# Kernel tuning notes

Measured on AMD Instinct MI355X. Metric: run time of the kernel, lower is better.

Reference implementation:

```python
import jax, jax.numpy as jnp
import numpy as np

N, D = 8192, 1024

def setup_inputs() -> dict:
    key = jax.random.key(0)
    ks = jax.random.split(key, 7)
    s = 1.0 / np.sqrt(D)
    return {
        "sent_mat": jax.random.normal(ks[0], (N, D), dtype=jnp.float32),
        "indicator": 0,
        "Wq": jax.random.normal(ks[1], (D, D), dtype=jnp.float32) * s,
        "bq": jax.random.normal(ks[2], (D,), dtype=jnp.float32) * s,
        "Wk": jax.random.normal(ks[3], (D, D), dtype=jnp.float32) * s,
        "bk": jax.random.normal(ks[4], (D,), dtype=jnp.float32) * s,
        "Wv": jax.random.normal(ks[5], (D, D), dtype=jnp.float32) * s,
        "bv": jax.random.normal(ks[6], (D,), dtype=jnp.float32) * s,
    }

def reference(sent_mat, indicator, Wq, bq, Wk, bk, Wv, bv):
    # torch.nn.Linear: y = x @ W.T + b
    Q = sent_mat @ Wq.T + bq            # [N, D]
    K = sent_mat @ Wk.T + bk            # [N, D]
    V = sent_mat @ Wv.T + bv            # [N, D]
    sim = Q @ K.T                       # [N, N]
    if indicator == 0:                  # custom score inversion
        sim = 1.0 - sim
    sim_norm = sim / jnp.sqrt(jnp.asarray(D, dtype=sim.dtype))
    # NOTE: softmax over dim=0 (columns normalized over rows), unconventional
    attn_w = jax.nn.softmax(sim_norm, axis=0)   # [N, N]
    attn_out = attn_w @ V               # [N, D]
    return (attn_out, attn_w)
```

## Files before the change

### kernel.cpp

```cpp
#include <hip/hip_runtime.h>

#define NT 8192
#define DM 1024

typedef unsigned short u16;
typedef __bf16 bf16x8 __attribute__((ext_vector_type(8)));
typedef float f32x4 __attribute__((ext_vector_type(4)));
typedef u16 u16x8 __attribute__((ext_vector_type(8)));

__device__ __forceinline__ u16 f2bf(float f) {
  union { float f; unsigned u; } v; v.f = f;
  unsigned r = v.u + 0x7fffu + ((v.u >> 16) & 1u);
  return (u16)(r >> 16);
}
__device__ __forceinline__ float bf2f(u16 h) {
  union { unsigned u; float f; } v; v.u = ((unsigned)h) << 16;
  return v.f;
}

__device__ __forceinline__ void stage16(const u16* g, u16* lds_wave_uniform) {
  __builtin_amdgcn_global_load_lds(
      (const __attribute__((address_space(1))) unsigned int*)g,
      (__attribute__((address_space(3))) unsigned int*)lds_wave_uniform, 16, 0, 0);
}

__global__ void cvt_all_kernel(const float* __restrict__ X, const float* __restrict__ Wq,
                               const float* __restrict__ Wk, const float* __restrict__ Wv,
                               u16* __restrict__ Xb, u16* __restrict__ Wqb,
                               u16* __restrict__ Wkb, u16* __restrict__ Wvb) {
  const int NX = NT * DM / 4;
  const int NW = DM * DM / 4;
  const int total = NX + 3 * NW;
  int i = blockIdx.x * blockDim.x + threadIdx.x;
  int stride = gridDim.x * blockDim.x;
  for (; i < total; i += stride) {
    const float* src; u16* dst; int j;
    if (i < NX)               { src = X;  dst = Xb;  j = i; }
    else if (i < NX + NW)     { src = Wq; dst = Wqb; j = i - NX; }
    else if (i < NX + 2 * NW) { src = Wk; dst = Wkb; j = i - NX - NW; }
    else                      { src = Wv; dst = Wvb; j = i - NX - 2 * NW; }
    float4 v = reinterpret_cast<const float4*>(src)[j];
    ushort4 o;
    o.x = f2bf(v.x); o.y = f2bf(v.y); o.z = f2bf(v.z); o.w = f2bf(v.w);
    reinterpret_cast<ushort4*>(dst)[j] = o;
  }
}

__global__ __launch_bounds__(512, 2)
void qkt_exp_256(const u16* __restrict__ Q, const u16* __restrict__ Kmat, int K, int lda,
                 u16* __restrict__ E, float* __restrict__ cs,
                 const int* __restrict__ indp) {
  __shared__ u16 AT[2][256 * 64];
  __shared__ u16 BT[2][256 * 64];
  const int t = threadIdx.x;
  const int l = t & 63;
  const int w = t >> 6;
  const int wm = w >> 2;
  const int wn = w & 3;
  const int r16 = l & 15;
  const int half = l >> 4;

  const int gx = gridDim.x;
  const int nwg = gx * gridDim.y;
  int lin = blockIdx.y * gx + blockIdx.x;
  if ((nwg & 7) == 0) lin = (lin & 7) * (nwg >> 3) + (lin >> 3);
  const int bx = lin % gx;
  const int by = lin / gx;
  const size_t brow = (size_t)by * 256;
  const size_t bcol = (size_t)bx * 256;

  const int srow = w * 8 + (l >> 3);
  const int kel = ((l & 7) ^ (l >> 3)) * 8;
  const int ntiles = K >> 6;

  f32x4 acc[8][4] = {};

#pragma unroll
  for (int q = 0; q < 4; ++q) {
    stage16(Q    + (brow + q * 64 + srow) * (size_t)lda + kel, &AT[0][q * 4096 + w * 512]);
    stage16(Kmat + (bcol + q * 64 + srow) * (size_t)lda + kel, &BT[0][q * 4096 + w * 512]);
  }
  __syncthreads();

  for (int tt = 0; tt < ntiles; ++tt) {
    const int cur = tt & 1;
    const int nxt = cur ^ 1;
    const int k1 = (tt + 1) << 6;
    const bool more = (tt + 1 < ntiles);
#pragma unroll
    for (int p = 0; p < 4; ++p) {
      if (p == 0 && more) {
#pragma unroll
        for (int q = 0; q < 4; ++q)
          stage16(Q + (brow + q * 64 + srow) * (size_t)lda + (k1 + kel),
                  &AT[nxt][q * 4096 + w * 512]);
      }
      if (p == 1 && more) {
#pragma unroll
        for (int q = 0; q < 4; ++q)
          stage16(Kmat + (bcol + q * 64 + srow) * (size_t)lda + (k1 + kel),
                  &BT[nxt][q * 4096 + w * 512]);
      }
      bf16x8 af[4][2], bfr[2][2];
#pragma unroll
      for (int m = 0; m < 4; ++m) {
        const int row = wm * 128 + (p >> 1) * 64 + m * 16 + r16;
#pragma unroll
        for (int kk = 0; kk < 2; ++kk) {
          const int slot = (half + 4 * kk) ^ (r16 & 7);
          af[m][kk] = *reinterpret_cast<const bf16x8*>(&AT[cur][row * 64 + slot * 8]);
        }
      }
#pragma unroll
      for (int n = 0; n < 2; ++n) {
        const int row = wn * 64 + (p & 1) * 32 + n * 16 + r16;
#pragma unroll
        for (int kk = 0; kk < 2; ++kk) {
          const int slot = (half + 4 * kk) ^ (r16 & 7);
          bfr[n][kk] = *reinterpret_cast<const bf16x8*>(&BT[cur][row * 64 + slot * 8]);
        }
      }
      __builtin_amdgcn_s_setprio(1);
#pragma unroll
      for (int m = 0; m < 4; ++m)
#pragma unroll
        for (int n = 0; n < 2; ++n)
#pragma unroll
          for (int kk = 0; kk < 2; ++kk)
            acc[(p >> 1) * 4 + m][(p & 1) * 2 + n] = __builtin_amdgcn_mfma_f32_16x16x32_bf16(
                af[m][kk], bfr[n][kk], acc[(p >> 1) * 4 + m][(p & 1) * 2 + n], 0, 0, 0);
      __builtin_amdgcn_s_setprio(0);
      __builtin_amdgcn_sched_barrier(0);
    }
    __syncthreads();
  }

  const bool flip = (*indp == 0);
  const float cexp = 0.045084220027780106f;
  float csum[4] = {0.f, 0.f, 0.f, 0.f};
#pragma unroll
  for (int mg = 0; mg < 8; ++mg) {
#pragma unroll
    for (int ng = 0; ng < 4; ++ng) {
#pragma unroll
      for (int q = 0; q < 4; ++q) {
        float s = acc[mg][ng][q];
        float x = flip ? (1.0f - s) : s;
        float e = exp2f(x * cexp);
        size_t row = brow + wm * 128 + mg * 16 + half * 4 + q;
        size_t col = bcol + wn * 64 + ng * 16 + r16;
        E[row * NT + col] = f2bf(e);
        csum[ng] += e;
      }
    }
  }
#pragma unroll
  for (int ng = 0; ng < 4; ++ng) {
    float s = csum[ng];
    s += __shfl_xor(s, 16);
    s += __shfl_xor(s, 32);
    if (l < 16) atomicAdd(&cs[bcol + wn * 64 + ng * 16 + l], s);
  }
}

template<int EPI>
__global__ __launch_bounds__(512, 4)
void mega_bt(const u16* __restrict__ A, const u16* __restrict__ B, int K,
             int lda, int ldb, int ldo,
             const float* __restrict__ b0, const float* __restrict__ b1,
             const float* __restrict__ csp,
             u16* __restrict__ obf, float* __restrict__ of32) {
  __shared__ u16 AT[3][128 * 32];
  __shared__ u16 BT[3][128 * 32];
  const int t = threadIdx.x;
  const int l = t & 63;
  const int w = t >> 6;
  const int wm = w >> 2;
  const int wn = w & 3;
  const int r16 = l & 15;
  const int half = l >> 4;

  const int gx = gridDim.x;
  const int nwg = gx * gridDim.y;
  int lin = blockIdx.y * gx + blockIdx.x;
  if ((nwg & 7) == 0) lin = (lin & 7) * (nwg >> 3) + (lin >> 3);
  const int bx = lin % gx;
  const int by = lin / gx;
  const size_t brow = (size_t)by * 128;
  const size_t bcol = (size_t)bx * 128;

  const int srow = w * 16 + (l >> 2);
  const int kel = (((l & 3) ^ ((l >> 2) & 3) ^ (((l >> 4) & 1) << 1))) * 8;
  const int nt = K >> 5;
  const int slotk = half ^ (r16 & 3) ^ (((r16 >> 2) & 1) << 1);

  f32x4 acc[4][2] = {};

#define STAGE(tile, buf)                                                              \
  {                                                                                   \
    const int k0_ = (tile) << 5;                                                      \
    stage16(A + (brow + srow) * (size_t)lda + (k0_ + kel), &AT[buf][w * 512]);        \
    stage16(B + (bcol + srow) * (size_t)ldb + (k0_ + kel), &BT[buf][w * 512]);        \
  }

  STAGE(0, 0);
  STAGE(1, 1);

  for (int tt = 0; tt < nt; ++tt) {
    const int cur = tt % 3;
    if (tt < nt - 1) asm volatile("s_waitcnt vmcnt(2)" ::: "memory");
    else             asm volatile("s_waitcnt vmcnt(0)" ::: "memory");
    __builtin_amdgcn_s_barrier();
    __builtin_amdgcn_sched_barrier(0);
    if (tt + 2 < nt) STAGE(tt + 2, (tt + 2) % 3);
    __builtin_amdgcn_sched_barrier(0);

    bf16x8 af[4], bfr[2];
#pragma unroll
    for (int m = 0; m < 4; ++m) {
      const int row = wm * 64 + m * 16 + r16;
      af[m] = *reinterpret_cast<const bf16x8*>(&AT[cur][row * 32 + slotk * 8]);
    }
#pragma unroll
    for (int n = 0; n < 2; ++n) {
      const int row = wn * 32 + n * 16 + r16;
      bfr[n] = *reinterpret_cast<const bf16x8*>(&BT[cur][row * 32 + slotk * 8]);
    }
    __builtin_amdgcn_s_setprio(1);
#pragma unroll
    for (int m = 0; m < 4; ++m)
#pragma unroll
      for (int n = 0; n < 2; ++n)
        acc[m][n] = __builtin_amdgcn_mfma_f32_16x16x32_bf16(af[m], bfr[n], acc[m][n], 0, 0, 0);
    __builtin_amdgcn_s_setprio(0);
  }
#undef STAGE

  if constexpr (EPI == 0) {
    const float* bp = ((bcol >> 10) == 0) ? b0 : b1;
#pragma unroll
    for (int mg = 0; mg < 4; ++mg) {
#pragma unroll
      for (int n = 0; n < 2; ++n) {
        const int cc = wn * 32 + n * 16 + r16;
        const float bv = bp[((int)bcol & 1023) + cc];
#pragma unroll
        for (int q = 0; q < 4; ++q) {
          size_t row = brow + wm * 64 + mg * 16 + half * 4 + q;
          obf[row * (size_t)ldo + bcol + cc] = f2bf(acc[mg][n][q] + bv);
        }
      }
    }
  } else if constexpr (EPI == 4) {
#pragma unroll
    for (int n = 0; n < 2; ++n) {
      const int cc = wn * 32 + n * 16 + r16;
      const float invc = 1.0f / csp[bcol + cc];
#pragma unroll
      for (int mg = 0; mg < 4; ++mg) {
#pragma unroll
        for (int q = 0; q < 4; ++q) {
          size_t row = brow + wm * 64 + mg * 16 + half * 4 + q;
          obf[row * (size_t)ldo + bcol + cc] = f2bf((acc[mg][n][q] + b0[row]) * invc);
        }
      }
    }
  } else {
#pragma unroll
    for (int mg = 0; mg < 4; ++mg) {
#pragma unroll
      for (int n = 0; n < 2; ++n) {
#pragma unroll
        for (int q = 0; q < 4; ++q) {
          size_t row = brow + wm * 64 + mg * 16 + half * 4 + q;
          size_t col = bcol + wn * 32 + n * 16 + r16;
          of32[row * (size_t)ldo + col] = acc[mg][n][q];
        }
      }
    }
  }
}

template<int EPI, int AF32, int BF32>
__global__ __launch_bounds__(256)
void gemm_bt(const void* __restrict__ Av, const void* __restrict__ Bv, int K, int ldo,
             const float* __restrict__ bias, u16* __restrict__ obf,
             float* __restrict__ of32, const int* __restrict__ indp) {
  __shared__ u16 As[128 * 32];
  __shared__ u16 Bs[128 * 32];
  const int t = threadIdx.x;
  const int l = t & 63;
  const int w = t >> 6;
  const int wr = w >> 1;
  const int wc = w & 1;
  const int r16 = l & 15;
  const int half = l >> 4;

  const int gx = gridDim.x;
  const int nwg = gx * gridDim.y;
  int lin = blockIdx.y * gx + blockIdx.x;
  if ((nwg & 7) == 0) lin = (lin & 7) * (nwg >> 3) + (lin >> 3);
  const int bx = lin % gx;
  const int by = lin / gx;

  const size_t brow = (size_t)by * 128;
  const size_t bcol = (size_t)bx * 128;
  const int kel = (l & 3) * 8;
  const int lrow = l >> 2;

  f32x4 acc[4][4] = {};

  for (int k0 = 0; k0 < K; k0 += 32) {
#pragma unroll
    for (int c = 0; c < 2; ++c) {
      const int seg = c * 4 + w;
      const int r = seg * 16 + lrow;
      if constexpr (AF32) {
        const float* ga = (const float*)Av + (brow + r) * (size_t)K + (k0 + kel);
        float4 u0 = *reinterpret_cast<const float4*>(ga);
        float4 u1 = *reinterpret_cast<const float4*>(ga + 4);
        u16x8 o;
        o[0] = f2bf(u0.x); o[1] = f2bf(u0.y); o[2] = f2bf(u0.z); o[3] = f2bf(u0.w);
        o[4] = f2bf(u1.x); o[5] = f2bf(u1.y); o[6] = f2bf(u1.z); o[7] = f2bf(u1.w);
        *reinterpret_cast<u16x8*>(&As[seg * 512 + l * 8]) = o;
      } else {
        const u16* ga = (const u16*)Av + (brow + r) * (size_t)K + (k0 + kel);
        stage16(ga, &As[seg * 512]);
      }
      if constexpr (BF32) {
        const float* gb = (const float*)Bv + (bcol + r) * (size_t)K + (k0 + kel);
        float4 u0 = *reinterpret_cast<const float4*>(gb);
        float4 u1 = *reinterpret_cast<const float4*>(gb + 4);
        u16x8 o;
        o[0] = f2bf(u0.x); o[1] = f2bf(u0.y); o[2] = f2bf(u0.z); o[3] = f2bf(u0.w);
        o[4] = f2bf(u1.x); o[5] = f2bf(u1.y); o[6] = f2bf(u1.z); o[7] = f2bf(u1.w);
        *reinterpret_cast<u16x8*>(&Bs[seg * 512 + l * 8]) = o;
      } else {
        const u16* gb = (const u16*)Bv + (bcol + r) * (size_t)K + (k0 + kel);
        stage16(gb, &Bs[seg * 512]);
      }
    }
    __syncthreads();
    bf16x8 af[4], bfv[4];
#pragma unroll
    for (int m = 0; m < 4; ++m)
      af[m] = *reinterpret_cast<const bf16x8*>(&As[(wr * 64 + m * 16 + r16) * 32 + half * 8]);
#pragma unroll
    for (int n = 0; n < 4; ++n)
      bfv[n] = *reinterpret_cast<const bf16x8*>(&Bs[(wc * 64 + n * 16 + r16) * 32 + half * 8]);
#pragma unroll
    for (int m = 0; m < 4; ++m)
#pragma unroll
      for (int n = 0; n < 4; ++n)
        acc[m][n] = __builtin_amdgcn_mfma_f32_16x16x32_bf16(af[m], bfv[n], acc[m][n], 0, 0, 0);
    __syncthreads();
  }

  const int crow0 = wr * 64 + half * 4;
  const int ccol0 = wc * 64 + r16;

  if constexpr (EPI == 0) {
#pragma unroll
    for (int m = 0; m < 4; ++m) {
#pragma unroll
      for (int n = 0; n < 4; ++n) {
        const int cc = ccol0 + n * 16;
        const float bv = bias[bcol + cc];
#pragma unroll
        for (int q = 0; q < 4; ++q) {
          size_t idx = (brow + crow0 + m * 16 + q) * (size_t)ldo + (bcol + cc);
          obf[idx] = f2bf(acc[m][n][q] + bv);
        }
      }
    }
  } else if constexpr (EPI == 1) {
    const bool flip = (*indp == 0);
    const float cexp = 0.045084220027780106f;
#pragma unroll
    for (int m = 0; m < 4; ++m) {
#pragma unroll
      for (int n = 0; n < 4; ++n) {
        const int cc = ccol0 + n * 16;
#pragma unroll
        for (int q = 0; q < 4; ++q) {
          float s = acc[m][n][q];
          float x = flip ? (1.0f - s) : s;
          size_t idx = (brow + crow0 + m * 16 + q) * (size_t)ldo + (bcol + cc);
          of32[idx] = exp2f(x * cexp);
        }
      }
    }
  } else {
#pragma unroll
    for (int m = 0; m < 4; ++m) {
#pragma unroll
      for (int n = 0; n < 4; ++n) {
        const int cc = ccol0 + n * 16;
#pragma unroll
        for (int q = 0; q < 4; ++q) {
          size_t idx = (brow + crow0 + m * 16 + q) * (size_t)ldo + (bcol + cc);
          of32[idx] = acc[m][n][q];
        }
      }
    }
  }
}

__global__ void colsum_kernel(const float* __restrict__ E, float* __restrict__ cs) {
  const int col = blockIdx.x * 256 + threadIdx.x;
  const int r0 = blockIdx.y * 256;
  float s = 0.f;
  for (int r = r0; r < r0 + 256; ++r)
    s += E[(size_t)r * NT + col];
  atomicAdd(&cs[col], s);
}

__global__ void norm_kernel(float* __restrict__ w, const float* __restrict__ cs, int n4) {
  int i = blockIdx.x * blockDim.x + threadIdx.x;
  int stride = gridDim.x * blockDim.x;
  for (; i < n4; i += stride) {
    float4 v = reinterpret_cast<float4*>(w)[i];
    int j4 = i & (NT / 4 - 1);
    float4 c = reinterpret_cast<const float4*>(cs)[j4];
    v.x /= c.x; v.y /= c.y; v.z /= c.z; v.w /= c.w;
    reinterpret_cast<float4*>(w)[i] = v;
  }
}

__global__ void norm_bf16_kernel(const u16* __restrict__ e, float* __restrict__ w,
                                 const float* __restrict__ cs, int n4) {
  int i = blockIdx.x * blockDim.x + threadIdx.x;
  int stride = gridDim.x * blockDim.x;
  for (; i < n4; i += stride) {
    ushort4 ev = reinterpret_cast<const ushort4*>(e)[i];
    int j4 = i & (NT / 4 - 1);
    float4 c = reinterpret_cast<const float4*>(cs)[j4];
    float4 v;
    v.x = bf2f(ev.x) / c.x;
    v.y = bf2f(ev.y) / c.y;
    v.z = bf2f(ev.z) / c.z;
    v.w = bf2f(ev.w) / c.w;
    reinterpret_cast<float4*>(w)[i] = v;
  }
}

__global__ void vt_kernel(const u16* __restrict__ Vb, const float* __restrict__ cs,
                          u16* __restrict__ Vt) {
  __shared__ u16 tile[64][65];
  const int jb = blockIdx.x * 64;
  const int db = blockIdx.y * 64;
  const int t = threadIdx.x;
  {
    const int d = t & 63;
    const int j0 = t >> 6;
    for (int jj = j0; jj < 64; jj += 4)
      tile[jj][d] = Vb[(size_t)(jb + jj) * DM + db + d];
  }
  __syncthreads();
  {
    const int j = t & 63;
    const int d0 = t >> 6;
    const float inv = cs ? (1.0f / cs[jb + j]) : 1.0f;
    for (int dd = d0; dd < 64; dd += 4) {
      u16 raw = tile[j][dd];
      Vt[(size_t)(db + dd) * NT + jb + j] = cs ? f2bf(bf2f(raw) * inv) : raw;
    }
  }
}

extern "C" void kernel_launch(void* const* d_in, const int* in_sizes, int n_in,
                              void* d_out, int out_size, void* d_ws, size_t ws_size,
                              hipStream_t stream) {
  const float* X  = (const float*)d_in[0];
  const int* indp = (const int*)d_in[1];
  const float* Wq = (const float*)d_in[2];
  const float* bq = (const float*)d_in[3];
  const float* Wk = (const float*)d_in[4];
  const float* bk = (const float*)d_in[5];
  const float* Wv = (const float*)d_in[6];
  const float* bv = (const float*)d_in[7];

  float* attn_out = (float*)d_out;
  float* attn_w   = (float*)d_out + (size_t)NT * DM;

  const size_t EB_BYTES = (size_t)NT * NT * 2;
  const size_t QKV_BYTES = (size_t)NT * DM * 2;
  const size_t need_fast = EB_BYTES + 4 * QKV_BYTES + NT * 4;

  if (ws_size >= need_fast) {
    char* ws = (char*)d_ws;
    u16* Eb  = (u16*)ws;
    u16* QKb = (u16*)(ws + EB_BYTES);
    u16* Vt  = QKb + (size_t)NT * 2048;
    u16* Xb  = Vt + (size_t)DM * NT;
    u16* Wvb = Xb + (size_t)NT * DM;
    float* cs = (float*)(Wvb + (size_t)DM * DM);
    u16* Wqkb = Eb;
    u16* Wqb = Wqkb;
    u16* Wkb = Wqkb + (size_t)DM * DM;

    cvt_all_kernel<<<2048, 256, 0, stream>>>(X, Wq, Wk, Wv, Xb, Wqb, Wkb, Wvb);

    mega_bt<0><<<dim3(2048 / 128, NT / 128), 512, 0, stream>>>(
        Xb, Wqkb, DM, DM, DM, 2048, bq, bk, nullptr, QKb, nullptr);

    hipMemsetAsync(cs, 0, NT * sizeof(float), stream);
    qkt_exp_256<<<dim3(NT / 256, NT / 256), 512, 0, stream>>>(
        QKb, QKb + 1024, DM, 2048, Eb, cs, indp);

    mega_bt<4><<<dim3(NT / 128, DM / 128), 512, 0, stream>>>(
        Wvb, Xb, DM, DM, DM, NT, bv, nullptr, cs, Vt, nullptr);

    mega_bt<2><<<dim3(DM / 128, NT / 128), 512, 0, stream>>>(
        Eb, Vt, NT, NT, NT, DM, nullptr, nullptr, nullptr, nullptr, attn_out);

    norm_bf16_kernel<<<4096, 256, 0, stream>>>(Eb, attn_w, cs, NT * NT / 4);
  } else {
    char* ws = (char*)d_ws;
    u16* Qb = (u16*)ws;  ws += QKV_BYTES;
    u16* Kb = (u16*)ws;  ws += QKV_BYTES;
    u16* Vb = (u16*)ws;  ws += QKV_BYTES;
    u16* Vt = (u16*)ws;  ws += QKV_BYTES;
    float* cs = (float*)ws;

    dim3 gqkv(DM / 128, NT / 128);
    gemm_bt<0, 1, 1><<<gqkv, 256, 0, stream>>>(X, Wq, DM, DM, bq, Qb, nullptr, nullptr);
    gemm_bt<0, 1, 1><<<gqkv, 256, 0, stream>>>(X, Wk, DM, DM, bk, Kb, nullptr, nullptr);
    gemm_bt<0, 1, 1><<<gqkv, 256, 0, stream>>>(X, Wv, DM, DM, bv, Vb, nullptr, nullptr);

    gemm_bt<1, 0, 0><<<dim3(NT / 128, NT / 128), 256, 0, stream>>>(
        Qb, Kb, DM, NT, nullptr, nullptr, attn_w, indp);

    hipMemsetAsync(cs, 0, NT * sizeof(float), stream);
    colsum_kernel<<<dim3(32, 32), 256, 0, stream>>>(attn_w, cs);
    norm_kernel<<<4096, 256, 0, stream>>>(attn_w, cs, NT * NT / 4);
    vt_kernel<<<dim3(NT / 64, DM / 64), 256, 0, stream>>>(Vb, nullptr, Vt);

    gemm_bt<2, 1, 0><<<dim3(DM / 128, NT / 128), 256, 0, stream>>>(
        attn_w, Vt, NT, DM, nullptr, nullptr, attn_out, nullptr);
  }
}
```

Measured before the change: 487.5 us.

## Use triple-buffered K=32 LDS tiles with vmcnt-based pipelining in QK^T kernel

Replaces the double-buffered 64-wide K tiles in the QK^T+exp kernel with three 32-wide K buffers, prefetching two tiles ahead. A single barrier per iteration is paired with explicit s_waitcnt vmcnt. The LDS swizzle is reworked for 32-element rows. The goal is deeper load/compute overlap and fewer synchronisations per byte loaded, at the cost of more loop iterations and fragile hand-tuned waitcnt counts.

Measured after the change: 519.5 us. +6.6%, slower.

```diff
diff --git a/kernel.cpp b/kernel.cpp
--- a/kernel.cpp
+++ b/kernel.cpp
@@ -50,8 +50,8 @@
 void qkt_exp_256(const u16* __restrict__ Q, const u16* __restrict__ Kmat, int K, int lda,
                  u16* __restrict__ E, float* __restrict__ cs,
                  const int* __restrict__ indp) {
-  __shared__ u16 AT[2][256 * 64];
-  __shared__ u16 BT[2][256 * 64];
+  __shared__ u16 AT[3][256 * 32];
+  __shared__ u16 BT[3][256 * 32];
   const int t = threadIdx.x;
   const int l = t & 63;
   const int w = t >> 6;
@@ -69,71 +69,58 @@
   const size_t brow = (size_t)by * 256;
   const size_t bcol = (size_t)bx * 256;
 
-  const int srow = w * 8 + (l >> 3);
-  const int kel = ((l & 7) ^ (l >> 3)) * 8;
-  const int ntiles = K >> 6;
+  const int srow = w * 16 + (l >> 2);
+  const int kel = (((l & 3) ^ ((l >> 2) & 3) ^ (((l >> 4) & 1) << 1))) * 8;
+  const int ntq = K >> 5;
+  const int slotk = half ^ (r16 & 3) ^ (((r16 >> 2) & 1) << 1);
 
   f32x4 acc[8][4] = {};
 
-#pragma unroll
-  for (int q = 0; q < 4; ++q) {
-    stage16(Q    + (brow + q * 64 + srow) * (size_t)lda + kel, &AT[0][q * 4096 + w * 512]);
-    stage16(Kmat + (bcol + q * 64 + srow) * (size_t)lda + kel, &BT[0][q * 4096 + w * 512]);
-  }
-  __syncthreads();
-
-  for (int tt = 0; tt < ntiles; ++tt) {
-    const int cur = tt & 1;
-    const int nxt = cur ^ 1;
-    const int k1 = (tt + 1) << 6;
-    const bool more = (tt + 1 < ntiles);
-#pragma unroll
-    for (int p = 0; p < 4; ++p) {
-      if (p == 0 && more) {
-#pragma unroll
-        for (int q = 0; q < 4; ++q)
-          stage16(Q + (brow + q * 64 + srow) * (size_t)lda + (k1 + kel),
-                  &AT[nxt][q * 4096 + w * 512]);
-      }
-      if (p == 1 && more) {
-#pragma unroll
-        for (int q = 0; q < 4; ++q)
-          stage16(Kmat + (bcol + q * 64 + srow) * (size_t)lda + (k1 + kel),
-                  &BT[nxt][q * 4096 + w * 512]);
-      }
-      bf16x8 af[4][2], bfr[2][2];
-#pragma unroll
-      for (int m = 0; m < 4; ++m) {
-        const int row = wm * 128 + (p >> 1) * 64 + m * 16 + r16;
-#pragma unroll
-        for (int kk = 0; kk < 2; ++kk) {
-          const int slot = (half + 4 * kk) ^ (r16 & 7);
-          af[m][kk] = *reinterpret_cast<const bf16x8*>(&AT[cur][row * 64 + slot * 8]);
-        }
-      }
-#pragma unroll
-      for (int n = 0; n < 2; ++n) {
-        const int row = wn * 64 + (p & 1) * 32 + n * 16 + r16;
-#pragma unroll
-        for (int kk = 0; kk < 2; ++kk) {
-          const int slot = (half + 4 * kk) ^ (r16 & 7);
-          bfr[n][kk] = *reinterpret_cast<const bf16x8*>(&BT[cur][row * 64 + slot * 8]);
-        }
-      }
-      __builtin_amdgcn_s_setprio(1);
-#pragma unroll
-      for (int m = 0; m < 4; ++m)
-#pragma unroll
-        for (int n = 0; n < 2; ++n)
-#pragma unroll
-          for (int kk = 0; kk < 2; ++kk)
-            acc[(p >> 1) * 4 + m][(p & 1) * 2 + n] = __builtin_amdgcn_mfma_f32_16x16x32_bf16(
-                af[m][kk], bfr[n][kk], acc[(p >> 1) * 4 + m][(p & 1) * 2 + n], 0, 0, 0);
-      __builtin_amdgcn_s_setprio(0);
-      __builtin_amdgcn_sched_barrier(0);
-    }
-    __syncthreads();
-  }
+#define QSTAGE(tile, buf)                                                             \
+  {                                                                                   \
+    const int k0_ = (tile) << 5;                                                      \
+    _Pragma("unroll")                                                                 \
+    for (int q = 0; q < 2; ++q)                                                       \
+      stage16(Q + (brow + q * 128 + srow) * (size_t)lda + (k0_ + kel),                \
+              &AT[buf][q * 4096 + w * 512]);                                          \
+    _Pragma("unroll")                                                                 \
+    for (int q = 0; q < 2; ++q)                                                       \
+      stage16(Kmat + (bcol + q * 128 + srow) * (size_t)lda + (k0_ + kel),             \
+              &BT[buf][q * 4096 + w * 512]);                                          \
+  }
+
+  QSTAGE(0, 0);
+  QSTAGE(1, 1);
+
+  for (int tt = 0; tt < ntq; ++tt) {
+    const int cur = tt % 3;
+    if (tt < ntq - 1) asm volatile("s_waitcnt vmcnt(4)" ::: "memory");
+    else              asm volatile("s_waitcnt vmcnt(0)" ::: "memory");
+    __builtin_amdgcn_s_barrier();
+    __builtin_amdgcn_sched_barrier(0);
+    if (tt + 2 < ntq) QSTAGE(tt + 2, (tt + 2) % 3);
+    __builtin_amdgcn_sched_barrier(0);
+
+    bf16x8 af[8], bfr[4];
+#pragma unroll
+    for (int m = 0; m < 8; ++m) {
+      const int row = wm * 128 + m * 16 + r16;
+      af[m] = *reinterpret_cast<const bf16x8*>(&AT[cur][row * 32 + slotk * 8]);
+    }
+#pragma unroll
+    for (int n = 0; n < 4; ++n) {
+      const int row = wn * 64 + n * 16 + r16;
+      bfr[n] = *reinterpret_cast<const bf16x8*>(&BT[cur][row * 32 + slotk * 8]);
+    }
+    __builtin_amdgcn_s_setprio(1);
+#pragma unroll
+    for (int m = 0; m < 8; ++m)
+#pragma unroll
+      for (int n = 0; n < 4; ++n)
+        acc[m][n] = __builtin_amdgcn_mfma_f32_16x16x32_bf16(af[m], bfr[n], acc[m][n], 0, 0, 0);
+    __builtin_amdgcn_s_setprio(0);
+  }
+#undef QSTAGE
 
   const bool flip = (*indp == 0);
   const float cexp = 0.045084220027780106f;
```
